# Performance work log

Measured on AMD Instinct MI355X. Metric: run time of the kernel, lower is better.

Reference implementation:

```python
import jax, jax.numpy as jnp
import numpy as np

B, H, W, C = 8, 64, 64, 512   # C = query_dim = text_dim
K = 256                        # text tokens
TOP_M = 5
EPS = 1e-5


def _ln(x, g, b):
    mu = jnp.mean(x, axis=-1, keepdims=True)
    var = jnp.var(x, axis=-1, keepdims=True)
    return (x - mu) / jnp.sqrt(var + EPS) * g + b


def setup_inputs() -> dict:
    key = jax.random.key(0)
    ks = jax.random.split(key, 10)
    s = 0.02
    return {
        "visual": jax.random.normal(ks[0], (B, H, W, C), jnp.float32),
        "text": jax.random.normal(ks[1], (B, K, C), jnp.float32),
        "g1": jnp.ones((C,), jnp.float32), "b1": jnp.zeros((C,), jnp.float32),
        "g2": jnp.ones((C,), jnp.float32), "b2": jnp.zeros((C,), jnp.float32),
        "Wq": jax.random.normal(ks[2], (C, C), jnp.float32) * s,   # query_dim -> text_dim
        "Wv": jax.random.normal(ks[3], (C, C), jnp.float32) * s,   # text_dim -> query_dim
        "logit_scale": jnp.asarray(np.log(1.0 / 0.07), jnp.float32),
        "Wg": jax.random.normal(ks[4], (C, 1), jnp.float32) * s,
        "bg": jnp.zeros((1,), jnp.float32),
        "W1": jax.random.normal(ks[5], (C, 4 * C), jnp.float32) * s,
        "bff1": jnp.zeros((4 * C,), jnp.float32),
        "W2": jax.random.normal(ks[6], (4 * C, C), jnp.float32) * s,
        "bff2": jnp.zeros((C,), jnp.float32),
    }


def reference(visual, text, g1, b1, g2, b2, Wq, Wv, logit_scale, Wg, bg, W1, bff1, W2, bff2):
    Bv, Hv, Wdim, Cv = visual.shape
    N = Hv * Wdim
    x = _ln(visual, g1, b1).reshape(Bv, N, Cv)           # (B,N,C) pre-LN
    q = x @ Wq                                            # (B,N,Ct)
    q = q / jnp.linalg.norm(q, axis=-1, keepdims=True)
    k = text / jnp.linalg.norm(text, axis=-1, keepdims=True)  # (B,K,Ct)
    v = text @ Wv                                         # (B,K,C)
    scale = jnp.exp(logit_scale) / jnp.sqrt(jnp.asarray(Cv, jnp.float32))
    sim = jnp.einsum('bnc,bkc->bnk', q, k) * scale        # (B,N,K)
    top_vals, top_idx = jax.lax.top_k(sim, TOP_M)         # (B,N,m)
    attn = jax.nn.softmax(top_vals, axis=-1)
    v_sel = jax.vmap(lambda vb, ib: vb[ib])(v, top_idx)   # (B,N,m,C) gather
    aligned = jnp.einsum('bnm,bnmc->bnc', attn, v_sel)    # weighted sum
    gate = jax.nn.sigmoid(x @ Wg + bg)                    # (B,N,1)
    aligned = aligned * gate
    y = x + aligned                                        # residual
    y = _ln(y, g2, b2)
    h = jax.nn.gelu(y @ W1 + bff1, approximate=False)
    y = y + (h @ W2 + bff2)
    return y.reshape(Bv, Hv, Wdim, Cv)
```

## Files before the change

### kernel.cpp

```cpp
#include <hip/hip_runtime.h>
#include <hip/hip_bf16.h>

typedef unsigned short u16;
typedef float f32x4 __attribute__((ext_vector_type(4)));
typedef short bf16x8 __attribute__((ext_vector_type(8)));

#define DEV __device__ __forceinline__

DEV float btof(u16 u) { return __uint_as_float(((unsigned)u) << 16); }
DEV u16 f2b(float f) {
  unsigned u = __float_as_uint(f);
  return (u16)((u + 0x7fffu + ((u >> 16) & 1u)) >> 16);
}
DEV void gld16(const void* g, void* l) {
  __builtin_amdgcn_global_load_lds(
      (const __attribute__((address_space(1))) void*)g,
      (__attribute__((address_space(3))) void*)l, 16, 0, 0);
}
DEV float gelu_fast(float x) {
  float xx = x * x;
  float u = x * fmaf(xx, 0.0356774081f, 0.7978845608f);
  u = fminf(fmaxf(u, -15.f), 15.f);
  float e = __expf(-2.0f * u);
  float d = 1.0f + e;
  float r; asm("v_rcp_f32 %0, %1" : "=v"(r) : "v"(d));
  float t = (1.0f - e) * r;
  return 0.5f * x * (1.0f + t);
}

template <int EPI>
__global__ __launch_bounds__(512, 2) void gemm256(
    const u16* __restrict__ A, long lda, const u16* __restrict__ B, long ldb,
    void* __restrict__ Cv, long ldc, int K, long sA, long sB, long sC,
    const float* __restrict__ aux1, const void* __restrict__ aux2)
{
  __shared__ u16 lds[2][16384];
  const int tid = threadIdx.x;
  const int lane = tid & 63, wid = tid >> 6;
  const int wm = wid >> 2, wn = wid & 3;
  const int qr = lane >> 4, qc = lane & 15;

  const int gx = gridDim.x, gy = gridDim.y;
  const int nwg = gx * gy * (int)gridDim.z;
  const int orig = blockIdx.x + gx * (blockIdx.y + gy * blockIdx.z);
  const int nid = (orig & 7) * (nwg >> 3) + (orig >> 3);
  const int bx = nid % gx;
  const int rem1 = nid / gx;
  const int by = rem1 % gy;
  const long z = rem1 / gy;

  const long m0 = (long)by << 8, n0 = (long)bx << 8;
  const u16* Ab = A + z * sA;
  const u16* Bb = B + z * sB;
  const int T = K >> 5;

  f32x4 acc[8][4];
#pragma unroll
  for (int m = 0; m < 8; ++m)
#pragma unroll
    for (int n = 0; n < 4; ++n) acc[m][n] = (f32x4){0.f, 0.f, 0.f, 0.f};

  const int c0 = wid * 128 + lane, c1 = c0 + 64;
  const int r0 = c0 >> 2, r1 = c1 >> 2;
  const int k0off = ((c0 & 3) ^ ((r0 >> 1) & 3)) << 3;
  const int k1off = ((c1 & 3) ^ ((r1 >> 1) & 3)) << 3;
  const u16* pa0 = Ab + (m0 + r0) * lda + k0off;
  const u16* pa1 = Ab + (m0 + r1) * lda + k1off;
  const u16* pb0 = Bb + (n0 + r0) * ldb + k0off;
  const u16* pb1 = Bb + (n0 + r1) * ldb + k1off;
  const int e0 = c0 * 8, e1 = c1 * 8;

  const int swz = (qr ^ ((qc >> 1) & 3)) << 3;

  auto ldA = [&](bf16x8* dst, int bsel, int mh) {
#pragma unroll
    for (int mm = 0; mm < 4; ++mm) {
      const int rr = wm * 128 + (mh * 4 + mm) * 16 + qc;
      dst[mm] = *(const bf16x8*)&lds[bsel][rr * 32 + swz];
    }
  };
  auto ldB = [&](bf16x8* dst, int bsel) {
#pragma unroll
    for (int n = 0; n < 4; ++n) {
      const int rr = wn * 64 + n * 16 + qc;
      dst[n] = *(const bf16x8*)&lds[bsel][8192 + rr * 32 + swz];
    }
  };

  gld16(pa0, &lds[0][e0]);        gld16(pa1, &lds[0][e1]);
  gld16(pb0, &lds[0][8192 + e0]); gld16(pb1, &lds[0][8192 + e1]);
  pa0 += 32; pa1 += 32; pb0 += 32; pb1 += 32;

#define MFMAQ(MB) \
    __builtin_amdgcn_s_setprio(1); \
    _Pragma("unroll") \
    for (int mm = 0; mm < 4; ++mm) \
      _Pragma("unroll") \
      for (int n = 0; n < 4; ++n) \
        acc[MB + mm][n] = __builtin_amdgcn_mfma_f32_16x16x32_bf16( \
            a4[mm], b4[n], acc[MB + mm][n], 0, 0, 0); \
    __builtin_amdgcn_s_setprio(0);

#define TILE32(BUF, PF, SO) { \
    bf16x8 a4[4], b4[4]; \
    if (PF) { gld16(pa0 + (SO), &lds[BUF ^ 1][e0]); \
              gld16(pa1 + (SO), &lds[BUF ^ 1][e1]); \
              gld16(pb0 + (SO), &lds[BUF ^ 1][8192 + e0]); \
              gld16(pb1 + (SO), &lds[BUF ^ 1][8192 + e1]); \
              asm volatile("s_waitcnt vmcnt(4)" ::: "memory"); } \
    else    { asm volatile("s_waitcnt vmcnt(0)" ::: "memory"); } \
    __builtin_amdgcn_s_barrier(); \
    ldA(a4, BUF, 0); ldB(b4, BUF); \
    MFMAQ(0) \
    ldA(a4, BUF, 1); \
    MFMAQ(4) \
    asm volatile("s_waitcnt lgkmcnt(0)" ::: "memory"); \
    __builtin_amdgcn_s_barrier(); }

  for (int t2 = 0; t2 < T; t2 += 2) {
    TILE32(0, true, 0)
    TILE32(1, (t2 + 2 < T), 32)
    pa0 += 64; pa1 += 64; pb0 += 64; pb1 += 64;
  }
#undef TILE32
#undef MFMAQ

  if constexpr (EPI == 6) {
    float* rsc2 = (float*)Cv;
#pragma unroll
    for (int m = 0; m < 8; ++m)
#pragma unroll
      for (int j = 0; j < 4; ++j) {
        float s = 0.f;
#pragma unroll
        for (int n = 0; n < 4; ++n) { float t2 = acc[m][n][j]; s = fmaf(t2, t2, s); }
        s += __shfl_xor(s, 1); s += __shfl_xor(s, 2);
        s += __shfl_xor(s, 4); s += __shfl_xor(s, 8);
        if (qc == 0)
          atomicAdd(rsc2 + (m0 + wm * 128 + m * 16 + qr * 4 + j), s);
      }
  } else {
#pragma unroll
    for (int m = 0; m < 8; ++m) {
#pragma unroll
      for (int n = 0; n < 4; ++n) {
        const long row0 = m0 + wm * 128 + m * 16 + qr * 4;
        const long col = n0 + wn * 64 + n * 16 + qc;
#pragma unroll
        for (int j = 0; j < 4; ++j) {
          const long idx = z * sC + (row0 + j) * ldc + col;
          float val = acc[m][n][j];
          if constexpr (EPI == 0) ((float*)Cv)[idx] = val;
          else if constexpr (EPI == 4)
            ((u16*)Cv)[idx] = f2b(gelu_fast(val + aux1[col]));
          else if constexpr (EPI == 5) {
            float r = btof(((const u16*)aux2)[idx]);
            ((float*)Cv)[idx] = val + aux1[col] + r;
          }
        }
      }
    }
  }
}

template <int EPI>
__global__ __launch_bounds__(256) void gemm_bt(
    const u16* __restrict__ A, long lda, const u16* __restrict__ B, long ldb,
    void* __restrict__ Cv, long ldc, int K)
{
  const int tid = threadIdx.x;
  const int lane = tid & 63, wv = tid >> 6;
  const int wr = wv >> 1, wc = wv & 1;
  const int m0 = blockIdx.y << 7, n0 = blockIdx.x << 7;

  __shared__ u16 lsA[128 * 64];
  __shared__ u16 lsB[128 * 64];

  f32x4 acc[4][4];
#pragma unroll
  for (int m = 0; m < 4; ++m)
#pragma unroll
    for (int n = 0; n < 4; ++n) acc[m][n] = (f32x4){0.f, 0.f, 0.f, 0.f};

  const int srow = tid >> 3;
  const int scol = (tid & 7) << 3;
  const int qr = lane >> 4, qc = lane & 15;

  for (int k0 = 0; k0 < K; k0 += 64) {
#pragma unroll
    for (int p = 0; p < 4; ++p) {
      gld16(A + (long)(m0 + (p << 5) + srow) * lda + k0 + scol,
            &lsA[(p * 4 + wv) * 512]);
      gld16(B + (long)(n0 + (p << 5) + srow) * ldb + k0 + scol,
            &lsB[(p * 4 + wv) * 512]);
    }
    __syncthreads();
#pragma unroll
    for (int kk = 0; kk < 64; kk += 32) {
      bf16x8 af[4], bfr[4];
#pragma unroll
      for (int m = 0; m < 4; ++m)
        af[m] = *(const bf16x8*)&lsA[(wr * 64 + m * 16 + qc) * 64 + kk + qr * 8];
#pragma unroll
      for (int n = 0; n < 4; ++n)
        bfr[n] = *(const bf16x8*)&lsB[(wc * 64 + n * 16 + qc) * 64 + kk + qr * 8];
#pragma unroll
      for (int m = 0; m < 4; ++m)
#pragma unroll
        for (int n = 0; n < 4; ++n)
          acc[m][n] = __builtin_amdgcn_mfma_f32_16x16x32_bf16(af[m], bfr[n],
                                                              acc[m][n], 0, 0, 0);
    }
    __syncthreads();
  }

#pragma unroll
  for (int m = 0; m < 4; ++m) {
#pragma unroll
    for (int n = 0; n < 4; ++n) {
      const int row0 = m0 + wr * 64 + m * 16 + qr * 4;
      const int col = n0 + wc * 64 + n * 16 + qc;
#pragma unroll
      for (int j = 0; j < 4; ++j) {
        const long idx = (long)(row0 + j) * ldc + col;
        if constexpr (EPI == 3) ((u16*)Cv)[idx] = f2b(acc[m][n][j]);
      }
    }
  }
}

__global__ __launch_bounds__(256) void transpose_bf16(
    const float* __restrict__ src, u16* __restrict__ dst, int R, int C)
{
  __shared__ float t[64][65];
  const int c0 = blockIdx.x * 64, r0 = blockIdx.y * 64;
  for (int j = threadIdx.y; j < 64; j += 4)
    t[j][threadIdx.x] = src[(long)(r0 + j) * C + c0 + threadIdx.x];
  __syncthreads();
  for (int j = threadIdx.y; j < 64; j += 4)
    dst[(long)(c0 + j) * R + r0 + threadIdx.x] = f2b(t[threadIdx.x][j]);
}

__global__ __launch_bounds__(256) void transpose_f32(
    const float* __restrict__ src, float* __restrict__ dst, int R, int C,
    long sS, long sD)
{
  __shared__ float t[64][65];
  const int c0 = blockIdx.x * 64, r0 = blockIdx.y * 64;
  const long z = blockIdx.z;
  for (int j = threadIdx.y; j < 64; j += 4)
    t[j][threadIdx.x] = src[z * sS + (long)(r0 + j) * C + c0 + threadIdx.x];
  __syncthreads();
  for (int j = threadIdx.y; j < 64; j += 4)
    dst[z * sD + (long)(c0 + j) * R + r0 + threadIdx.x] = t[threadIdx.x][j];
}

__global__ __launch_bounds__(256) void ln1_kernel(
    const float* __restrict__ vis, const float* __restrict__ g1,
    const float* __restrict__ b1, const float* __restrict__ Wg,
    const float* __restrict__ bg, u16* __restrict__ x3,
    u16* __restrict__ xr2, float* __restrict__ gate)
{
  const int lane = threadIdx.x & 63, wv = threadIdx.x >> 6;
  const long row = (long)blockIdx.x * 4 + wv;
  const float* src = vis + row * 512 + lane * 8;
  float v[8];
  *(float4*)&v[0] = *(const float4*)src;
  *(float4*)&v[4] = *(const float4*)(src + 4);
  float s = 0.f, sq = 0.f;
#pragma unroll
  for (int j = 0; j < 8; ++j) { s += v[j]; sq += v[j] * v[j]; }
#pragma unroll
  for (int off = 32; off; off >>= 1) { s += __shfl_xor(s, off); sq += __shfl_xor(sq, off); }
  const float mu = s * (1.f / 512.f);
  const float var = sq * (1.f / 512.f) - mu * mu;
  const float rstd = 1.0f / sqrtf(var + 1e-5f);

  float g1r[8], b1r[8], wgr[8];
  *(float4*)&g1r[0] = *(const float4*)(g1 + lane * 8);
  *(float4*)&g1r[4] = *(const float4*)(g1 + lane * 8 + 4);
  *(float4*)&b1r[0] = *(const float4*)(b1 + lane * 8);
  *(float4*)&b1r[4] = *(const float4*)(b1 + lane * 8 + 4);
  *(float4*)&wgr[0] = *(const float4*)(Wg + lane * 8);
  *(float4*)&wgr[4] = *(const float4*)(Wg + lane * 8 + 4);

  bf16x8 p0, p1, p2;
  float gd = 0.f;
#pragma unroll
  for (int j = 0; j < 8; ++j) {
    float d = (v[j] - mu) * rstd * g1r[j] + b1r[j];
    gd += d * wgr[j];
    u16 h0 = f2b(d);        float r1 = d - btof(h0);
    u16 h1 = f2b(r1);       float r2 = r1 - btof(h1);
    u16 h2 = f2b(r2);
    p0[j] = (short)h0; p1[j] = (short)h1; p2[j] = (short)h2;
  }
#pragma unroll
  for (int off = 32; off; off >>= 1) gd += __shfl_xor(gd, off);
  if (lane == 0) gate[row] = 1.0f / (1.0f + __expf(-(gd + bg[0])));

  u16* dst = x3 + row * 1536 + lane * 8;
  *(bf16x8*)dst = p0;
  *(bf16x8*)(dst + 512) = p1;
  *(bf16x8*)(dst + 1024) = p0;
  *(bf16x8*)(xr2 + row * 512 + lane * 8) = p2;
}

__global__ __launch_bounds__(256) void knorm_kernel(
    const float* __restrict__ text, float* __restrict__ kn, u16* __restrict__ tb)
{
  const int lane = threadIdx.x & 63, wv = threadIdx.x >> 6;
  const long row = (long)blockIdx.x * 4 + wv;
  const float* src = text + row * 512 + lane * 8;
  float v[8];
  *(float4*)&v[0] = *(const float4*)src;
  *(float4*)&v[4] = *(const float4*)(src + 4);
  float sq = 0.f;
#pragma unroll
  for (int j = 0; j < 8; ++j) sq += v[j] * v[j];
#pragma unroll
  for (int off = 32; off; off >>= 1) sq += __shfl_xor(sq, off);
  const float nrm = sqrtf(sq);
  float kv[8];
  bf16x8 pt;
#pragma unroll
  for (int j = 0; j < 8; ++j) { kv[j] = v[j] / nrm; pt[j] = (short)f2b(v[j]); }
  float* kd = kn + row * 512 + lane * 8;
  *(float4*)kd = *(float4*)&kv[0];
  *(float4*)(kd + 4) = *(float4*)&kv[4];
  *(bf16x8*)(tb + row * 512 + lane * 8) = pt;
}

__global__ __launch_bounds__(256) void wtilde_kernel(
    const float* __restrict__ Wq, const float* __restrict__ kT,
    double* __restrict__ wtmp)
{
  const int c0 = blockIdx.x * 4;
  const int b = blockIdx.y;
  __shared__ float wrow[4][512];
#pragma unroll
  for (int i = 0; i < 8; ++i) {
    int idx = threadIdx.x + i * 256;
    wrow[idx >> 9][idx & 511] = Wq[(long)c0 * 512 + idx];
  }
  __syncthreads();
  const int k = threadIdx.x;
  const float* kTb = kT + (long)b * 512 * 256 + k;
  double a0 = 0, a1 = 0, a2 = 0, a3 = 0;
  for (int j = 0; j < 512; ++j) {
    double kvd = (double)kTb[(long)j * 256];
    a0 += (double)wrow[0][j] * kvd;
    a1 += (double)wrow[1][j] * kvd;
    a2 += (double)wrow[2][j] * kvd;
    a3 += (double)wrow[3][j] * kvd;
  }
  double* o = wtmp + ((long)b * 512 + c0) * 256 + k;
  o[0] = a0; o[256] = a1; o[512] = a2; o[768] = a3;
}

__global__ __launch_bounds__(256) void wtilde_split(
    const double* __restrict__ wtmp, u16* __restrict__ wA,
    double* __restrict__ wtmpT)
{
  __shared__ double t[64][65];
  const int t0 = blockIdx.x * 64, c0 = blockIdx.y * 64, b = blockIdx.z;
  const double* s = wtmp + (long)b * 512 * 256;
  for (int j = threadIdx.y; j < 64; j += 4)
    t[j][threadIdx.x] = s[(long)(c0 + j) * 256 + t0 + threadIdx.x];
  __syncthreads();
  for (int j = threadIdx.y; j < 64; j += 4) {
    double wv = t[threadIdx.x][j];
    u16 h0 = f2b((float)wv);  double r1 = wv - (double)btof(h0);
    u16 h1 = f2b((float)r1);
    const long kb = (long)b * 256 + t0 + j;
    const int c = c0 + threadIdx.x;
    wA[kb * 1536 + c] = h0;
    wA[kb * 1536 + 512 + c] = h0;
    wA[kb * 1536 + 1024 + c] = h1;
    wtmpT[kb * 512 + c] = wv;
  }
}

__global__ __launch_bounds__(256) void qfinish_kernel(
    const float* __restrict__ rsc2, const float* __restrict__ ls,
    float* __restrict__ rsc)
{
  const int i = blockIdx.x * 256 + threadIdx.x;
  rsc[i] = __expf(ls[0]) * 0.044194173824159223f * rsqrtf(rsc2[i]);
}

__global__ __launch_bounds__(256) void topk_fuse(
    const float* __restrict__ sim, const u16* __restrict__ v,
    const u16* __restrict__ x3, const u16* __restrict__ xr2,
    const float* __restrict__ gate, const double* __restrict__ wtmpT,
    const float* __restrict__ rsc, const float* __restrict__ g2,
    const float* __restrict__ b2, u16* __restrict__ yb)
{
  const int lane = threadIdx.x & 63, wv = threadIdx.x >> 6;
  const long row = (long)blockIdx.x * 4 + wv;
  const int b = (int)(row >> 12);

  const u16* xr = x3 + row * 1536 + lane * 8;
  bf16x8 a0 = *(const bf16x8*)xr;
  bf16x8 a1 = *(const bf16x8*)(xr + 512);
  float xv[8];
#pragma unroll
  for (int j = 0; j < 8; ++j) xv[j] = btof((u16)a0[j]) + btof((u16)a1[j]);

  float4 sv = *(const float4*)(sim + row * 256 + lane * 4);
  float vals[4] = {sv.x, sv.y, sv.z, sv.w};
  float topv[8]; int topi[8];
#pragma unroll
  for (int m = 0; m < 8; ++m) {
    float bv = vals[0]; int bl = 0;
    if (vals[1] > bv) { bv = vals[1]; bl = 1; }
    if (vals[2] > bv) { bv = vals[2]; bl = 2; }
    if (vals[3] > bv) { bv = vals[3]; bl = 3; }
    int bi = lane * 4 + bl;
#pragma unroll
    for (int off = 32; off; off >>= 1) {
      float ov = __shfl_xor(bv, off);
      int oi = __shfl_xor(bi, off);
      if (ov > bv || (ov == bv && oi < bi)) { bv = ov; bi = oi; }
    }
    topv[m] = bv; topi[m] = bi;
    if ((bi >> 2) == lane) {
      int tt = bi & 3;
      if (tt == 0) vals[0] = -INFINITY; else if (tt == 1) vals[1] = -INFINITY;
      else if (tt == 2) vals[2] = -INFINITY; else vals[3] = -INFINITY;
    }
  }

  if (topv[4] - topv[5] < 2e-4f) {
    bf16x8 a2 = *(const bf16x8*)(xr2 + row * 512 + lane * 8);
    double xd[8];
#pragma unroll
    for (int j = 0; j < 8; ++j)
      xd[j] = (double)btof((u16)a0[j]) + (double)btof((u16)a1[j]) +
              (double)btof((u16)a2[j]);
    double cv[8]; int ti[8];
#pragma unroll
    for (int m = 0; m < 8; ++m) {
      const double* wp = wtmpT + ((long)b * 256 + topi[m]) * 512 + lane * 8;
      double a = 0.0;
#pragma unroll
      for (int j = 0; j < 8; ++j) a += xd[j] * wp[j];
#pragma unroll
      for (int off = 32; off; off >>= 1) a += __shfl_xor(a, off);
      cv[m] = a; ti[m] = topi[m];
    }
#define CE(i, jj) { \
    bool sw = (cv[jj] > cv[i]) || (cv[jj] == cv[i] && ti[jj] < ti[i]); \
    double tv = cv[i]; int tix = ti[i]; \
    cv[i] = sw ? cv[jj] : cv[i];  ti[i] = sw ? ti[jj] : ti[i]; \
    cv[jj] = sw ? tv : cv[jj];    ti[jj] = sw ? tix : ti[jj]; }
    CE(0,1) CE(2,3) CE(4,5) CE(6,7)
    CE(0,2) CE(1,3) CE(4,6) CE(5,7)
    CE(1,2) CE(5,6)
    CE(0,4) CE(1,5) CE(2,6) CE(3,7)
    CE(2,4) CE(3,5)
    CE(1,2) CE(3,4) CE(5,6)
#undef CE
#pragma unroll
    for (int m = 0; m < 5; ++m) { topv[m] = (float)cv[m]; topi[m] = ti[m]; }
  }

  const float rs = rsc[row];
  float e[5], se = 0.f;
#pragma unroll
  for (int m = 0; m < 5; ++m) {
    e[m] = __expf((topv[m] - topv[0]) * rs); se += e[m];
  }
  const float inv = 1.0f / se;
  const float g = gate[row];

  float acc8[8] = {0, 0, 0, 0, 0, 0, 0, 0};
#pragma unroll
  for (int m = 0; m < 5; ++m) {
    const u16* vr = v + ((long)b * 256 + topi[m]) * 512 + lane * 8;
    bf16x8 vv = *(const bf16x8*)vr;
    float wgt = e[m] * inv;
#pragma unroll
    for (int j = 0; j < 8; ++j) acc8[j] += wgt * btof((u16)vv[j]);
  }

  float y8[8]; float s = 0.f, sq = 0.f;
#pragma unroll
  for (int j = 0; j < 8; ++j) {
    y8[j] = xv[j] + acc8[j] * g;
    s += y8[j]; sq += y8[j] * y8[j];
  }
#pragma unroll
  for (int off = 32; off; off >>= 1) { s += __shfl_xor(s, off); sq += __shfl_xor(sq, off); }
  const float mu = s * (1.f / 512.f);
  const float var = sq * (1.f / 512.f) - mu * mu;
  const float rstd = 1.0f / sqrtf(var + 1e-5f);

  float g2r[8], b2r[8];
  *(float4*)&g2r[0] = *(const float4*)(g2 + lane * 8);
  *(float4*)&g2r[4] = *(const float4*)(g2 + lane * 8 + 4);
  *(float4*)&b2r[0] = *(const float4*)(b2 + lane * 8);
  *(float4*)&b2r[4] = *(const float4*)(b2 + lane * 8 + 4);
  bf16x8 outp;
#pragma unroll
  for (int j = 0; j < 8; ++j)
    outp[j] = (short)f2b((y8[j] - mu) * rstd * g2r[j] + b2r[j]);
  *(bf16x8*)(yb + row * 512 + lane * 8) = outp;
}

extern "C" void kernel_launch(void* const* d_in, const int* in_sizes, int n_in,
                              void* d_out, int out_size, void* d_ws,
                              size_t ws_size, hipStream_t stream)
{
  const float* vis  = (const float*)d_in[0];
  const float* text = (const float*)d_in[1];
  const float* g1   = (const float*)d_in[2];
  const float* b1   = (const float*)d_in[3];
  const float* g2   = (const float*)d_in[4];
  const float* b2   = (const float*)d_in[5];
  const float* Wq   = (const float*)d_in[6];
  const float* Wv   = (const float*)d_in[7];
  const float* ls   = (const float*)d_in[8];
  const float* Wg   = (const float*)d_in[9];
  const float* bg   = (const float*)d_in[10];
  const float* W1   = (const float*)d_in[11];
  const float* bff1 = (const float*)d_in[12];
  const float* W2   = (const float*)d_in[13];
  const float* bff2 = (const float*)d_in[14];
  (void)in_sizes; (void)n_in; (void)out_size; (void)ws_size;

  char* w = (char*)d_ws;
  auto alloc = [&](size_t bytes) {
    char* p = w; w += (bytes + 255) & ~(size_t)255; return p;
  };
  u16* x3 = (u16*)alloc(134217728);
  u16* h = x3;
  char* gap = (char*)x3 + 100663296;
  double* wtmp = (double*)gap;
  double* wtmpT = (double*)(gap + 8388608);
  u16* wA = (u16*)(gap + 16777216);
  float* sim = (float*)alloc(33554432);
  u16* yb = (u16*)alloc(33554432);
  u16* xr2 = (u16*)alloc(33554432);
  float* kn = (float*)alloc(4194304);
  float* kT = (float*)alloc(4194304);
  u16* tb = (u16*)alloc(2097152);
  u16* vb = (u16*)alloc(2097152);
  u16* WqT = (u16*)alloc(524288);
  u16* WvT = (u16*)alloc(524288);
  u16* W1T = (u16*)alloc(2097152);
  u16* W2T = (u16*)alloc(2097152);
  float* gate = (float*)alloc(131072);
  float* rsc = (float*)alloc(131072);
  float* rsc2 = (float*)alloc(131072);

  dim3 b256(256), b512(512), bT(64, 4);

  transpose_bf16<<<dim3(8, 8), bT, 0, stream>>>(Wq, WqT, 512, 512);
  transpose_bf16<<<dim3(8, 8), bT, 0, stream>>>(Wv, WvT, 512, 512);
  transpose_bf16<<<dim3(32, 8), bT, 0, stream>>>(W1, W1T, 512, 2048);
  transpose_bf16<<<dim3(8, 32), bT, 0, stream>>>(W2, W2T, 2048, 512);

  ln1_kernel<<<8192, b256, 0, stream>>>(vis, g1, b1, Wg, bg, x3, xr2, gate);
  knorm_kernel<<<512, b256, 0, stream>>>(text, kn, tb);
  transpose_f32<<<dim3(8, 4, 8), bT, 0, stream>>>(kn, kT, 256, 512,
                                                  256L * 512, 256L * 512);
  wtilde_kernel<<<dim3(128, 8), b256, 0, stream>>>(Wq, kT, wtmp);
  wtilde_split<<<dim3(4, 8, 8), bT, 0, stream>>>(wtmp, wA, wtmpT);

  hipMemsetAsync(rsc2, 0, 131072, stream);
  gemm256<6><<<dim3(2, 128, 1), b512, 0, stream>>>(x3, 1536, WqT, 512, rsc2,
                                                   1, 512, 0, 0, 0, nullptr,
                                                   nullptr);
  qfinish_kernel<<<128, b256, 0, stream>>>(rsc2, ls, rsc);

  gemm_bt<3><<<dim3(4, 16, 1), b256, 0, stream>>>(tb, 512, WvT, 512, vb, 512,
                                                  512);

  gemm256<0><<<dim3(1, 16, 8), b512, 0, stream>>>(
      x3, 1536, wA, 1536, sim, 256, 1536, 4096L * 1536, 256L * 1536,
      4096L * 256, nullptr, nullptr);

  topk_fuse<<<8192, b256, 0, stream>>>(sim, vb, x3, xr2, gate, wtmpT, rsc, g2,
                                       b2, yb);

  gemm256<4><<<dim3(8, 128, 1), b512, 0, stream>>>(yb, 512, W1T, 512, h, 2048,
                                                   512, 0, 0, 0, bff1,
                                                   nullptr);
  gemm256<5><<<dim3(2, 128, 1), b512, 0, stream>>>(h, 2048, W2T, 2048, d_out,
                                                   512, 2048, 0, 0, 0, bff2,
                                                   yb);
}
```

Measured before the change: 439.4 us.

## Deepen GEMM LDS pipeline to four stages and fuse small launch kernels

The bf16 GEMM moves from a two-buffer to a four-buffer LDS ring, keeping two K-tiles of global-to-LDS loads in flight with matching vmcnt waits. The aim is to hide more global-load latency behind the MFMA work. The price is a 128KB LDS footprint per block, which may not allow the two blocks per CU that the launch bounds ask for. Three smaller changes also reduce overhead: GELU becomes a sigmoid form built on v_exp_f32 and v_rcp_f32, the four weight transposes run as one launch, and the qfinish kernel is folded into topk_fuse.

```diff
diff --git a/kernel.cpp b/kernel.cpp
--- a/kernel.cpp
+++ b/kernel.cpp
@@ -19,13 +19,10 @@
 }
 DEV float gelu_fast(float x) {
   float xx = x * x;
-  float u = x * fmaf(xx, 0.0356774081f, 0.7978845608f);
-  u = fminf(fmaxf(u, -15.f), 15.f);
-  float e = __expf(-2.0f * u);
-  float d = 1.0f + e;
-  float r; asm("v_rcp_f32 %0, %1" : "=v"(r) : "v"(d));
-  float t = (1.0f - e) * r;
-  return 0.5f * x * (1.0f + t);
+  float p = fmaf(xx, -0.10294357f, -2.3022077f);
+  float e; asm("v_exp_f32 %0, %1" : "=v"(e) : "v"(p * x));
+  float r; asm("v_rcp_f32 %0, %1" : "=v"(r) : "v"(1.0f + e));
+  return x * r;
 }
 
 template <int EPI>
@@ -34,7 +31,7 @@
     void* __restrict__ Cv, long ldc, int K, long sA, long sB, long sC,
     const float* __restrict__ aux1, const void* __restrict__ aux2)
 {
-  __shared__ u16 lds[2][16384];
+  __shared__ u16 lds[4][16384];
   const int tid = threadIdx.x;
   const int lane = tid & 63, wid = tid >> 6;
   const int wm = wid >> 2, wn = wid & 3;
@@ -89,7 +86,9 @@
 
   gld16(pa0, &lds[0][e0]);        gld16(pa1, &lds[0][e1]);
   gld16(pb0, &lds[0][8192 + e0]); gld16(pb1, &lds[0][8192 + e1]);
-  pa0 += 32; pa1 += 32; pb0 += 32; pb1 += 32;
+  gld16(pa0 + 32, &lds[1][e0]);        gld16(pa1 + 32, &lds[1][e1]);
+  gld16(pb0 + 32, &lds[1][8192 + e0]); gld16(pb1 + 32, &lds[1][8192 + e1]);
+  pa0 += 64; pa1 += 64; pb0 += 64; pb1 += 64;
 
 #define MFMAQ(MB) \
     __builtin_amdgcn_s_setprio(1); \
@@ -101,13 +100,14 @@
             a4[mm], b4[n], acc[MB + mm][n], 0, 0, 0); \
     __builtin_amdgcn_s_setprio(0);
 
-#define TILE32(BUF, PF, SO) { \
+#define TILE32(BUF, PF1, PF2, SO) { \
     bf16x8 a4[4], b4[4]; \
-    if (PF) { gld16(pa0 + (SO), &lds[BUF ^ 1][e0]); \
-              gld16(pa1 + (SO), &lds[BUF ^ 1][e1]); \
-              gld16(pb0 + (SO), &lds[BUF ^ 1][8192 + e0]); \
-              gld16(pb1 + (SO), &lds[BUF ^ 1][8192 + e1]); \
-              asm volatile("s_waitcnt vmcnt(4)" ::: "memory"); } \
+    if (PF2) { gld16(pa0 + (SO), &lds[(BUF + 2) & 3][e0]); \
+               gld16(pa1 + (SO), &lds[(BUF + 2) & 3][e1]); \
+               gld16(pb0 + (SO), &lds[(BUF + 2) & 3][8192 + e0]); \
+               gld16(pb1 + (SO), &lds[(BUF + 2) & 3][8192 + e1]); \
+               asm volatile("s_waitcnt vmcnt(8)" ::: "memory"); } \
+    else if (PF1) { asm volatile("s_waitcnt vmcnt(4)" ::: "memory"); } \
     else    { asm volatile("s_waitcnt vmcnt(0)" ::: "memory"); } \
     __builtin_amdgcn_s_barrier(); \
     ldA(a4, BUF, 0); ldB(b4, BUF); \
@@ -117,10 +117,13 @@
     asm volatile("s_waitcnt lgkmcnt(0)" ::: "memory"); \
     __builtin_amdgcn_s_barrier(); }
 
-  for (int t2 = 0; t2 < T; t2 += 2) {
-    TILE32(0, true, 0)
-    TILE32(1, (t2 + 2 < T), 32)
-    pa0 += 64; pa1 += 64; pb0 += 64; pb1 += 64;
+  for (int t2 = 0; t2 < T; t2 += 4) {
+    const bool pfn = (t2 + 4 < T);
+    TILE32(0, true, true, 0)
+    TILE32(1, true, true, 32)
+    TILE32(2, true, pfn, 64)
+    TILE32(3, pfn, pfn, 96)
+    pa0 += 128; pa1 += 128; pb0 += 128; pb1 += 128;
   }
 #undef TILE32
 #undef MFMAQ
@@ -229,11 +232,20 @@
   }
 }
 
-__global__ __launch_bounds__(256) void transpose_bf16(
-    const float* __restrict__ src, u16* __restrict__ dst, int R, int C)
-{
+__global__ __launch_bounds__(256) void transpose_all(
+    const float* __restrict__ Wq, const float* __restrict__ Wv,
+    const float* __restrict__ W1, const float* __restrict__ W2,
+    u16* __restrict__ WqT, u16* __restrict__ WvT,
+    u16* __restrict__ W1T, u16* __restrict__ W2T)
+{
+  const int bid = blockIdx.x;
+  const float* src; u16* dst; int R, C, id, tilesX;
+  if (bid < 64)       { src = Wq; dst = WqT; R = 512;  C = 512;  id = bid;      tilesX = 8; }
+  else if (bid < 128) { src = Wv; dst = WvT; R = 512;  C = 512;  id = bid - 64; tilesX = 8; }
+  else if (bid < 384) { src = W1; dst = W1T; R = 512;  C = 2048; id = bid - 128; tilesX = 32; }
+  else                { src = W2; dst = W2T; R = 2048; C = 512;  id = bid - 384; tilesX = 8; }
+  const int c0 = (id % tilesX) * 64, r0 = (id / tilesX) * 64;
   __shared__ float t[64][65];
-  const int c0 = blockIdx.x * 64, r0 = blockIdx.y * 64;
   for (int j = threadIdx.y; j < 64; j += 4)
     t[j][threadIdx.x] = src[(long)(r0 + j) * C + c0 + threadIdx.x];
   __syncthreads();
@@ -381,20 +393,13 @@
   }
 }
 
-__global__ __launch_bounds__(256) void qfinish_kernel(
-    const float* __restrict__ rsc2, const float* __restrict__ ls,
-    float* __restrict__ rsc)
-{
-  const int i = blockIdx.x * 256 + threadIdx.x;
-  rsc[i] = __expf(ls[0]) * 0.044194173824159223f * rsqrtf(rsc2[i]);
-}
-
 __global__ __launch_bounds__(256) void topk_fuse(
     const float* __restrict__ sim, const u16* __restrict__ v,
     const u16* __restrict__ x3, const u16* __restrict__ xr2,
     const float* __restrict__ gate, const double* __restrict__ wtmpT,
-    const float* __restrict__ rsc, const float* __restrict__ g2,
-    const float* __restrict__ b2, u16* __restrict__ yb)
+    const float* __restrict__ rsc2, const float* __restrict__ ls,
+    const float* __restrict__ g2, const float* __restrict__ b2,
+    u16* __restrict__ yb)
 {
   const int lane = threadIdx.x & 63, wv = threadIdx.x >> 6;
   const long row = (long)blockIdx.x * 4 + wv;
@@ -465,7 +470,7 @@
     for (int m = 0; m < 5; ++m) { topv[m] = (float)cv[m]; topi[m] = ti[m]; }
   }
 
-  const float rs = rsc[row];
+  const float rs = __expf(ls[0]) * 0.044194173824159223f * rsqrtf(rsc2[row]);
   float e[5], se = 0.f;
 #pragma unroll
   for (int m = 0; m < 5; ++m) {
@@ -551,15 +556,11 @@
   u16* W1T = (u16*)alloc(2097152);
   u16* W2T = (u16*)alloc(2097152);
   float* gate = (float*)alloc(131072);
-  float* rsc = (float*)alloc(131072);
   float* rsc2 = (float*)alloc(131072);
 
   dim3 b256(256), b512(512), bT(64, 4);
 
-  transpose_bf16<<<dim3(8, 8), bT, 0, stream>>>(Wq, WqT, 512, 512);
-  transpose_bf16<<<dim3(8, 8), bT, 0, stream>>>(Wv, WvT, 512, 512);
-  transpose_bf16<<<dim3(32, 8), bT, 0, stream>>>(W1, W1T, 512, 2048);
-  transpose_bf16<<<dim3(8, 32), bT, 0, stream>>>(W2, W2T, 2048, 512);
+  transpose_all<<<640, bT, 0, stream>>>(Wq, Wv, W1, W2, WqT, WvT, W1T, W2T);
 
   ln1_kernel<<<8192, b256, 0, stream>>>(vis, g1, b1, Wg, bg, x3, xr2, gate);
   knorm_kernel<<<512, b256, 0, stream>>>(text, kn, tb);
@@ -572,7 +573,6 @@
   gemm256<6><<<dim3(2, 128, 1), b512, 0, stream>>>(x3, 1536, WqT, 512, rsc2,
                                                    1, 512, 0, 0, 0, nullptr,
                                                    nullptr);
-  qfinish_kernel<<<128, b256, 0, stream>>>(rsc2, ls, rsc);
 
   gemm_bt<3><<<dim3(4, 16, 1), b256, 0, stream>>>(tb, 512, WvT, 512, vb, 512,
                                                   512);
@@ -581,8 +581,8 @@
       x3, 1536, wA, 1536, sim, 256, 1536, 4096L * 1536, 256L * 1536,
       4096L * 256, nullptr, nullptr);
 
-  topk_fuse<<<8192, b256, 0, stream>>>(sim, vb, x3, xr2, gate, wtmpT, rsc, g2,
-                                       b2, yb);
+  topk_fuse<<<8192, b256, 0, stream>>>(sim, vb, x3, xr2, gate, wtmpT, rsc2,
+                                       ls, g2, b2, yb);
 
   gemm256<4><<<dim3(8, 128, 1), b512, 0, stream>>>(yb, 512, W1T, 512, h, 2048,
                                                    512, 0, 0, 0, bff1,
```

Result: no change. 431.2 us (-1.9%).
